# Performance work log

Measured on AMD Instinct MI355X. Metric: run time of the kernel, lower is better.

## Reference

```python
import jax, jax.numpy as jnp
import numpy as np

EPS = 1e-8

def setup_inputs() -> dict:
    key = jax.random.key(0)
    kx, kw = jax.random.split(key)
    B, T, C = 2048, 16384, 8
    x = jax.random.normal(kx, (B, T, C), dtype=jnp.float32)
    W = jax.random.normal(kw, (1, 5 * C), dtype=jnp.float32) * 0.1
    b = jnp.zeros((1,), dtype=jnp.float32)
    return {"x": x, "W": W, "b": b}

def _features(x):
    # x: [B, T, C]; compute 5 stats per channel, vectorized over all channels
    B, T, C = x.shape
    mean = jnp.mean(x, axis=1)                       # [B, C]
    # torch .std() default is unbiased (ddof=1)
    std = jnp.std(x, axis=1, ddof=1)                 # [B, C]
    centered = x - mean[:, None, :]
    skew = jnp.mean(centered ** 3, axis=1) / (std + EPS) ** 3
    mx = jnp.max(x, axis=1)                          # [B, C]
    cnt = jnp.sum(x > 0, axis=1).astype(x.dtype)     # [B, C]
    std_f = jnp.nan_to_num(std, nan=0.0)
    skew = jnp.nan_to_num(skew, nan=0.0)
    # torch stacks features channel-major: [max, mean, count, std, skew] per channel
    feats = jnp.stack([mx, mean, cnt, std_f, skew], axis=2)  # [B, C, 5]
    return feats.reshape(B, C * 5)                   # [B, 40]

def reference(x, W, b):
    feats = _features(x)
    return feats @ W.T + b                           # [B, 1]
```

## Files before the change

### kernel.cpp

```cpp
#include <hip/hip_runtime.h>
#include <math.h>

#define CCH 8
#define BLK 256

__global__ __launch_bounds__(BLK) void stats_dot_kernel(
    const float* __restrict__ x,
    const float* __restrict__ W,
    const float* __restrict__ bias,
    float* __restrict__ out,
    int T)
{
    const int b   = blockIdx.x;
    const int tid = threadIdx.x;
    const float* xb = x + (size_t)b * (size_t)T * CCH;

    float s1[CCH], s2[CCH], s3[CCH], mx[CCH];
    int   cnt[CCH];
#pragma unroll
    for (int c = 0; c < CCH; ++c) {
        s1[c] = 0.f; s2[c] = 0.f; s3[c] = 0.f;
        mx[c] = -INFINITY; cnt[c] = 0;
    }

    for (int t = tid; t < T; t += BLK) {
        const float4* p = (const float4*)(xb + (size_t)t * CCH);
        float4 v0 = p[0];
        float4 v1 = p[1];
        float v[8] = {v0.x, v0.y, v0.z, v0.w, v1.x, v1.y, v1.z, v1.w};
#pragma unroll
        for (int c = 0; c < CCH; ++c) {
            float xv = v[c];
            s1[c] += xv;
            s2[c]  = fmaf(xv, xv, s2[c]);
            s3[c]  = fmaf(xv * xv, xv, s3[c]);
            mx[c]  = fmaxf(mx[c], xv);
            cnt[c] += (xv > 0.f) ? 1 : 0;
        }
    }

    double d1[CCH], d2[CCH], d3[CCH];
#pragma unroll
    for (int c = 0; c < CCH; ++c) { d1[c] = s1[c]; d2[c] = s2[c]; d3[c] = s3[c]; }

#pragma unroll
    for (int off = 32; off >= 1; off >>= 1) {
#pragma unroll
        for (int c = 0; c < CCH; ++c) {
            d1[c] += __shfl_down(d1[c], off);
            d2[c] += __shfl_down(d2[c], off);
            d3[c] += __shfl_down(d3[c], off);
            mx[c]  = fmaxf(mx[c], __shfl_down(mx[c], off));
            cnt[c] += __shfl_down(cnt[c], off);
        }
    }

    __shared__ double sh1[4][CCH], sh2[4][CCH], sh3[4][CCH];
    __shared__ float  shm[4][CCH];
    __shared__ int    shc[4][CCH];

    const int wave = tid >> 6;
    const int lane = tid & 63;
    if (lane == 0) {
#pragma unroll
        for (int c = 0; c < CCH; ++c) {
            sh1[wave][c] = d1[c];
            sh2[wave][c] = d2[c];
            sh3[wave][c] = d3[c];
            shm[wave][c] = mx[c];
            shc[wave][c] = cnt[c];
        }
    }
    __syncthreads();

    if (tid == 0) {
        const double Td = (double)T;
        float result = bias[0];
#pragma unroll
        for (int c = 0; c < CCH; ++c) {
            double S1 = 0.0, S2 = 0.0, S3 = 0.0;
            float  M  = -INFINITY;
            int    CT = 0;
#pragma unroll
            for (int w = 0; w < 4; ++w) {
                S1 += sh1[w][c]; S2 += sh2[w][c]; S3 += sh3[w][c];
                M = fmaxf(M, shm[w][c]); CT += shc[w][c];
            }
            double m1  = S1 / Td;
            double var = (S2 - S1 * m1) / (Td - 1.0);
            if (var < 0.0) var = 0.0;
            double sd  = sqrt(var);
            double m2  = S2 / Td;
            double m3  = S3 / Td;
            double c3  = m3 - 3.0 * m1 * m2 + 2.0 * m1 * m1 * m1;
            double sde = sd + 1e-8;
            double skew = c3 / (sde * sde * sde);
            result += M          * W[c * 5 + 0];
            result += (float)m1  * W[c * 5 + 1];
            result += (float)CT  * W[c * 5 + 2];
            result += (float)sd  * W[c * 5 + 3];
            result += (float)skew* W[c * 5 + 4];
        }
        out[b] = result;
    }
}

extern "C" void kernel_launch(void* const* d_in, const int* in_sizes, int n_in,
                              void* d_out, int out_size, void* d_ws, size_t ws_size,
                              hipStream_t stream) {
    const float* x  = (const float*)d_in[0];
    const float* W  = (const float*)d_in[1];
    const float* bi = (const float*)d_in[2];
    float* out = (float*)d_out;

    const int B = out_size;
    const int T = in_sizes[0] / (B * CCH);

    stats_dot_kernel<<<B, BLK, 0, stream>>>(x, W, bi, out, T);
}
```

Baseline: 201.8 us.

## Use one float4 per thread with nontemporal loads and float wave reductions

Each thread now loads a single 16-byte vector per iteration, so even and odd lanes handle channels 0-3 and 4-7. This halves per-thread register state, makes the loads fully contiguous across the wave, and uses nontemporal loads with a 4x unroll to keep more memory requests in flight. The wave reduction switches from double to float shuffles, stops at offset 2 to keep the two channel groups apart, and stores per-group partials to shared memory. Launch bounds now request higher occupancy. The price is lower precision in the partial sums (float rather than double across lanes), which could slightly affect the skew and std accuracy.

```diff
diff --git a/kernel.cpp b/kernel.cpp
--- a/kernel.cpp
+++ b/kernel.cpp
@@ -4,7 +4,9 @@
 #define CCH 8
 #define BLK 256
 
-__global__ __launch_bounds__(BLK) void stats_dot_kernel(
+typedef float f32x4 __attribute__((ext_vector_type(4)));
+
+__global__ __launch_bounds__(BLK, 8) void stats_dot_kernel(
     const float* __restrict__ x,
     const float* __restrict__ W,
     const float* __restrict__ bias,
@@ -13,23 +15,22 @@
 {
     const int b   = blockIdx.x;
     const int tid = threadIdx.x;
-    const float* xb = x + (size_t)b * (size_t)T * CCH;
+    const f32x4* xb = (const f32x4*)(x + (size_t)b * (size_t)T * CCH);
+    const int nvec = T * 2;
 
-    float s1[CCH], s2[CCH], s3[CCH], mx[CCH];
-    int   cnt[CCH];
+    float s1[4], s2[4], s3[4], mx[4];
+    int   cnt[4];
 #pragma unroll
-    for (int c = 0; c < CCH; ++c) {
+    for (int c = 0; c < 4; ++c) {
         s1[c] = 0.f; s2[c] = 0.f; s3[c] = 0.f;
         mx[c] = -INFINITY; cnt[c] = 0;
     }
 
-    for (int t = tid; t < T; t += BLK) {
-        const float4* p = (const float4*)(xb + (size_t)t * CCH);
-        float4 v0 = p[0];
-        float4 v1 = p[1];
-        float v[8] = {v0.x, v0.y, v0.z, v0.w, v1.x, v1.y, v1.z, v1.w};
+#pragma unroll 4
+    for (int j = tid; j < nvec; j += BLK) {
+        f32x4 v = __builtin_nontemporal_load(xb + j);
 #pragma unroll
-        for (int c = 0; c < CCH; ++c) {
+        for (int c = 0; c < 4; ++c) {
             float xv = v[c];
             s1[c] += xv;
             s2[c]  = fmaf(xv, xv, s2[c]);
@@ -39,36 +40,30 @@
         }
     }
 
-    double d1[CCH], d2[CCH], d3[CCH];
 #pragma unroll
-    for (int c = 0; c < CCH; ++c) { d1[c] = s1[c]; d2[c] = s2[c]; d3[c] = s3[c]; }
-
+    for (int off = 32; off >= 2; off >>= 1) {
 #pragma unroll
-    for (int off = 32; off >= 1; off >>= 1) {
-#pragma unroll
-        for (int c = 0; c < CCH; ++c) {
-            d1[c] += __shfl_down(d1[c], off);
-            d2[c] += __shfl_down(d2[c], off);
-            d3[c] += __shfl_down(d3[c], off);
+        for (int c = 0; c < 4; ++c) {
+            s1[c] += __shfl_down(s1[c], off);
+            s2[c] += __shfl_down(s2[c], off);
+            s3[c] += __shfl_down(s3[c], off);
             mx[c]  = fmaxf(mx[c], __shfl_down(mx[c], off));
             cnt[c] += __shfl_down(cnt[c], off);
         }
     }
 
-    __shared__ double sh1[4][CCH], sh2[4][CCH], sh3[4][CCH];
-    __shared__ float  shm[4][CCH];
-    __shared__ int    shc[4][CCH];
-
+    __shared__ float sh[4][2][4][5];
     const int wave = tid >> 6;
     const int lane = tid & 63;
-    if (lane == 0) {
+    if (lane < 2) {
+        const int g = lane;
 #pragma unroll
-        for (int c = 0; c < CCH; ++c) {
-            sh1[wave][c] = d1[c];
-            sh2[wave][c] = d2[c];
-            sh3[wave][c] = d3[c];
-            shm[wave][c] = mx[c];
-            shc[wave][c] = cnt[c];
+        for (int c = 0; c < 4; ++c) {
+            sh[wave][g][c][0] = mx[c];
+            sh[wave][g][c][1] = s1[c];
+            sh[wave][g][c][2] = (float)cnt[c];
+            sh[wave][g][c][3] = s2[c];
+            sh[wave][g][c][4] = s3[c];
         }
     }
     __syncthreads();
@@ -77,14 +72,17 @@
         const double Td = (double)T;
         float result = bias[0];
 #pragma unroll
-        for (int c = 0; c < CCH; ++c) {
-            double S1 = 0.0, S2 = 0.0, S3 = 0.0;
+        for (int ch = 0; ch < CCH; ++ch) {
+            const int g = ch >> 2, c = ch & 3;
+            double S1 = 0.0, S2 = 0.0, S3 = 0.0, CT = 0.0;
             float  M  = -INFINITY;
-            int    CT = 0;
 #pragma unroll
             for (int w = 0; w < 4; ++w) {
-                S1 += sh1[w][c]; S2 += sh2[w][c]; S3 += sh3[w][c];
-                M = fmaxf(M, shm[w][c]); CT += shc[w][c];
+                M   = fmaxf(M, sh[w][g][c][0]);
+                S1 += (double)sh[w][g][c][1];
+                CT += (double)sh[w][g][c][2];
+                S2 += (double)sh[w][g][c][3];
+                S3 += (double)sh[w][g][c][4];
             }
             double m1  = S1 / Td;
             double var = (S2 - S1 * m1) / (Td - 1.0);
@@ -95,11 +93,11 @@
             double c3  = m3 - 3.0 * m1 * m2 + 2.0 * m1 * m1 * m1;
             double sde = sd + 1e-8;
             double skew = c3 / (sde * sde * sde);
-            result += M          * W[c * 5 + 0];
-            result += (float)m1  * W[c * 5 + 1];
-            result += (float)CT  * W[c * 5 + 2];
-            result += (float)sd  * W[c * 5 + 3];
-            result += (float)skew* W[c * 5 + 4];
+            result += M           * W[ch * 5 + 0];
+            result += (float)m1   * W[ch * 5 + 1];
+            result += (float)CT   * W[ch * 5 + 2];
+            result += (float)sd   * W[ch * 5 + 3];
+            result += (float)skew * W[ch * 5 + 4];
         }
         out[b] = result;
     }
```

Result: faster. 163.8 us (-18.8%).
